# Kernel optimization log

Measured on AMD Instinct MI355X. Metric: run time of the kernel, lower is better.

The kernel has to match this reference:

```python
import jax, jax.numpy as jnp
import numpy as np

HIDDEN = 768  # hidden_dim of the embedding matrix
VOCAB = 30522


def setup_inputs() -> dict:
    key = jax.random.key(0)
    k1, k2, k3, k4, k5, k6 = jax.random.split(key, 6)
    core = jax.random.normal(k1, (40, 256, 256), dtype=jnp.float32)
    f0 = jax.random.normal(k2, (40, 40), dtype=jnp.float32)
    f1 = jax.random.normal(k3, (768, 256), dtype=jnp.float32)
    f2 = jax.random.normal(k4, (768, 256), dtype=jnp.float32)
    ids = jax.random.randint(k5, (8192,), 0, VOCAB, dtype=jnp.int32)
    x = jax.random.normal(k6, (8192, 768), dtype=jnp.float32)  # unused by forward, kept for signature parity
    return {"x": x, "ids": ids, "core": core, "f0": f0, "f1": f1, "f2": f2}


def reference(x, ids, core, f0, f1, f2):
    # tucker_to_tensor: core x_0 f0 x_1 f1 x_2 f2 -> (40, 768, 768)
    res = jnp.einsum('abc,ia,jb,kc->ijk', core, f0, f1, f2)
    # flatten to padded embedding table (30720, 768) and gather requested rows
    table = res.reshape(-1, HIDDEN)
    return table[ids, :]
```

## Files before the change

kernel.cpp:

```cpp
#include <hip/hip_runtime.h>


#define A_DIM 40
#define BC 65536
#define C_DIM 256
#define HID 768

typedef __attribute__((ext_vector_type(8))) short short8;
typedef __attribute__((ext_vector_type(4))) float floatx4;

#define AS1 __attribute__((address_space(1)))
#define AS3 __attribute__((address_space(3)))

__device__ __forceinline__ void gl2lds16(const unsigned short* g, unsigned short* l) {
    __builtin_amdgcn_global_load_lds((const AS1 unsigned int*)g, (AS3 unsigned int*)l,
                                     16, 0, 0);
}

__device__ __forceinline__ unsigned short f2bf(float f) {
    unsigned int u = __builtin_bit_cast(unsigned int, f);
    u += 0x7FFFu + ((u >> 16) & 1u);
    return (unsigned short)(u >> 16);
}

__global__ __launch_bounds__(256) void k01_fused(const float* __restrict__ core,
                                                 const float* __restrict__ f0,
                                                 const float* __restrict__ f1,
                                                 const float* __restrict__ f2,
                                                 unsigned short* __restrict__ A1t,
                                                 unsigned short* __restrict__ f1b,
                                                 unsigned short* __restrict__ f2b) {
    const int bid = blockIdx.x;
    const int tid = threadIdx.x;
    if (bid < 512) {
        __shared__ float f0s[200];
        __shared__ unsigned short tt[32 * 34];
        const int i0 = (bid >> 6) * 5;
        const int tile = bid & 63;
        const int b0 = (tile >> 3) * 32;
        const int c0 = (tile & 7) * 32;
        if (tid < 200) f0s[tid] = f0[i0 * A_DIM + tid];
        __syncthreads();

        const int pb = (tid >> 4) * 2;
        const int pc = (tid & 15) * 2;
        float acc[5][4];
#pragma unroll
        for (int ii = 0; ii < 5; ++ii)
#pragma unroll
            for (int e = 0; e < 4; ++e) acc[ii][e] = 0.f;

        const float* cp0 = core + (b0 + pb) * 256 + (c0 + pc);
        for (int a = 0; a < A_DIM; ++a) {
            const float* cp = cp0 + a * BC;
            const float2 r0 = *(const float2*)cp;
            const float2 r1 = *(const float2*)(cp + 256);
#pragma unroll
            for (int ii = 0; ii < 5; ++ii) {
                const float fa = f0s[ii * A_DIM + a];
                acc[ii][0] += fa * r0.x;
                acc[ii][1] += fa * r0.y;
                acc[ii][2] += fa * r1.x;
                acc[ii][3] += fa * r1.y;
            }
        }
        const int rc = tid >> 3;
        const int rb4 = (tid & 7) * 4;
#pragma unroll
        for (int ii = 0; ii < 5; ++ii) {
            if (ii) __syncthreads();
            unsigned short e00 = f2bf(acc[ii][0]);
            unsigned short e10 = f2bf(acc[ii][2]);
            unsigned short e01 = f2bf(acc[ii][1]);
            unsigned short e11 = f2bf(acc[ii][3]);
            *(unsigned int*)&tt[pc * 34 + pb]       = (unsigned int)e00 | ((unsigned int)e10 << 16);
            *(unsigned int*)&tt[(pc + 1) * 34 + pb] = (unsigned int)e01 | ((unsigned int)e11 << 16);
            __syncthreads();
            unsigned short o[4];
#pragma unroll
            for (int u = 0; u < 4; ++u) o[u] = tt[rc * 34 + rb4 + u];
            unsigned int lo = (unsigned int)o[0] | ((unsigned int)o[1] << 16);
            unsigned int hi = (unsigned int)o[2] | ((unsigned int)o[3] << 16);
            *(uint2*)&A1t[(size_t)(i0 + ii) * BC + (c0 + rc) * 256 + b0 + rb4] = make_uint2(lo, hi);
        }
    } else {
        const int idx = (bid - 512) * 256 + tid;
        const float* src;
        unsigned short* dst;
        int off;
        if (idx < 49152) { src = f1; dst = f1b; off = idx; }
        else             { src = f2; dst = f2b; off = idx - 49152; }
        const float4 v = *(const float4*)&src[off * 4];
        const unsigned int lo = (unsigned int)f2bf(v.x) | ((unsigned int)f2bf(v.y) << 16);
        const unsigned int hi = (unsigned int)f2bf(v.z) | ((unsigned int)f2bf(v.w) << 16);
        *(uint2*)&dst[off * 4] = make_uint2(lo, hi);
    }
}

__global__ __launch_bounds__(256) void k2_gemm(const unsigned short* __restrict__ f1b,
                                               const unsigned short* __restrict__ A1t,
                                               unsigned short* __restrict__ A2) {
    const int j0  = blockIdx.x * 128;
    const int cb0 = blockIdx.y * 128;

    __shared__ unsigned short As[128 * 32];
    __shared__ unsigned short Bs[128 * 32];

    const int tid = threadIdx.x;
    const int lane = tid & 63, wave = tid >> 6;
    const int wm = (wave >> 1) * 64, wn = (wave & 1) * 64;
    const int l16 = lane & 15, q = lane >> 4;

    floatx4 acc[4][4];
#pragma unroll
    for (int p = 0; p < 4; ++p)
#pragma unroll
        for (int r = 0; r < 4; ++r) acc[p][r] = (floatx4)0.f;

    for (int kk = 0; kk < C_DIM; kk += 32) {
#pragma unroll
        for (int u = 0; u < 2; ++u) {
            const int chunk = (wave * 2 + u) * 64 + lane;
            const int row = chunk >> 2;
            const int sl  = (chunk & 3) * 8;
            gl2lds16(&f1b[(j0 + row) * 256 + kk + sl],                 &As[(wave * 2 + u) * 512]);
            gl2lds16(&A1t[(size_t)(cb0 + row) * 256 + kk + sl],        &Bs[(wave * 2 + u) * 512]);
        }
        __syncthreads();
        short8 af[4], bf[4];
#pragma unroll
        for (int p = 0; p < 4; ++p) af[p] = *(const short8*)&As[(wm + p * 16 + l16) * 32 + q * 8];
#pragma unroll
        for (int r = 0; r < 4; ++r) bf[r] = *(const short8*)&Bs[(wn + r * 16 + l16) * 32 + q * 8];
#pragma unroll
        for (int p = 0; p < 4; ++p)
#pragma unroll
            for (int r = 0; r < 4; ++r)
                acc[p][r] = __builtin_amdgcn_mfma_f32_16x16x32_bf16(af[p], bf[r], acc[p][r], 0, 0, 0);
        __syncthreads();
    }
#pragma unroll
    for (int p = 0; p < 4; ++p)
#pragma unroll
        for (int r = 0; r < 4; ++r) {
            const int col = cb0 + wn + r * 16 + l16;
            const size_t base = (size_t)(col >> 8) * (768 * 256) + (size_t)(col & 255);
#pragma unroll
            for (int rr = 0; rr < 4; ++rr) {
                const int row = j0 + wm + p * 16 + q * 4 + rr;
                A2[base + (size_t)row * 256] = f2bf(acc[p][r][rr]);
            }
        }
}

__global__ __launch_bounds__(256) void k3_gemm(const unsigned short* __restrict__ A2,
                                               const unsigned short* __restrict__ f2b,
                                               const int* __restrict__ ids,
                                               float* __restrict__ out) {
    const int n0 = blockIdx.x * 128;
    const int k0 = blockIdx.y * 128;

    __shared__ int ids_s[128];
    __shared__ unsigned short As[128 * 32];
    __shared__ unsigned short Bs[128 * 32];

    const int tid = threadIdx.x;
    if (tid < 128) ids_s[tid] = ids[n0 + tid];
    __syncthreads();

    const int lane = tid & 63, wave = tid >> 6;
    const int wm = (wave >> 1) * 64, wn = (wave & 1) * 64;
    const int l16 = lane & 15, q = lane >> 4;

    floatx4 acc[4][4];
#pragma unroll
    for (int p = 0; p < 4; ++p)
#pragma unroll
        for (int r = 0; r < 4; ++r) acc[p][r] = (floatx4)0.f;

    for (int kk = 0; kk < C_DIM; kk += 32) {
#pragma unroll
        for (int u = 0; u < 2; ++u) {
            const int chunk = (wave * 2 + u) * 64 + lane;
            const int row = chunk >> 2;
            const int sl  = (chunk & 3) * 8;
            gl2lds16(&A2[(size_t)ids_s[row] * 256 + kk + sl],   &As[(wave * 2 + u) * 512]);
            gl2lds16(&f2b[(k0 + row) * 256 + kk + sl],          &Bs[(wave * 2 + u) * 512]);
        }
        __syncthreads();
        short8 af[4], bf[4];
#pragma unroll
        for (int p = 0; p < 4; ++p) af[p] = *(const short8*)&As[(wm + p * 16 + l16) * 32 + q * 8];
#pragma unroll
        for (int r = 0; r < 4; ++r) bf[r] = *(const short8*)&Bs[(wn + r * 16 + l16) * 32 + q * 8];
#pragma unroll
        for (int p = 0; p < 4; ++p)
#pragma unroll
            for (int r = 0; r < 4; ++r)
                acc[p][r] = __builtin_amdgcn_mfma_f32_16x16x32_bf16(af[p], bf[r], acc[p][r], 0, 0, 0);
        __syncthreads();
    }
#pragma unroll
    for (int p = 0; p < 4; ++p)
#pragma unroll
        for (int r = 0; r < 4; ++r)
#pragma unroll
            for (int rr = 0; rr < 4; ++rr) {
                const int row = n0 + wm + p * 16 + q * 4 + rr;
                const int col = k0 + wn + r * 16 + l16;
                out[(size_t)row * HID + col] = acc[p][r][rr];
            }
}

extern "C" void kernel_launch(void* const* d_in, const int* in_sizes, int n_in,
                              void* d_out, int out_size, void* d_ws, size_t ws_size,
                              hipStream_t stream) {
    const int*   ids  = (const int*)d_in[1];
    const float* core = (const float*)d_in[2];
    const float* f0   = (const float*)d_in[3];
    const float* f1   = (const float*)d_in[4];
    const float* f2   = (const float*)d_in[5];
    float* out = (float*)d_out;

    char* ws = (char*)d_ws;
    unsigned short* A1t = (unsigned short*)ws;
    unsigned short* A2  = (unsigned short*)(ws + 5242880);
    unsigned short* f1b = (unsigned short*)(ws + 20971520);
    unsigned short* f2b = (unsigned short*)(ws + 21364736);

    k01_fused<<<896, 256, 0, stream>>>(core, f0, f1, f2, A1t, f1b, f2b);
    k2_gemm<<<dim3(6, 80), 256, 0, stream>>>(f1b, A1t, A2);
    k3_gemm<<<dim3(64, 6), 256, 0, stream>>>(A2, f2b, ids, out);
}
```

Before: 112.0 us.

## Double-buffer LDS tiles with async prefetch in both bf16 GEMM kernels

Both MFMA GEMM kernels (k2_gemm and k3_gemm) now keep two LDS buffers per operand. The next K-slice is issued via global_load_lds while MFMAs run on the current slice. The per-iteration pair of __syncthreads is replaced by one vmcnt(0) wait plus an s_barrier, the loop is fully unrolled, and global addresses (including the id-gathered rows in k3) are precomputed once. This is meant to hide global-load latency behind compute, at the cost of doubling the LDS footprint, which may reduce occupancy.

```diff
diff --git a/kernel.cpp b/kernel.cpp
--- a/kernel.cpp
+++ b/kernel.cpp
@@ -21,6 +21,12 @@
     unsigned int u = __builtin_bit_cast(unsigned int, f);
     u += 0x7FFFu + ((u >> 16) & 1u);
     return (unsigned short)(u >> 16);
+}
+
+__device__ __forceinline__ void dma_barrier() {
+    asm volatile("s_waitcnt vmcnt(0)" ::: "memory");
+    __builtin_amdgcn_s_barrier();
+    __builtin_amdgcn_sched_barrier(0);
 }
 
 __global__ __launch_bounds__(256) void k01_fused(const float* __restrict__ core,
@@ -103,42 +109,56 @@
     const int j0  = blockIdx.x * 128;
     const int cb0 = blockIdx.y * 128;
 
-    __shared__ unsigned short As[128 * 32];
-    __shared__ unsigned short Bs[128 * 32];
+    __shared__ unsigned short As[2][128 * 32];
+    __shared__ unsigned short Bs[2][128 * 32];
 
     const int tid = threadIdx.x;
     const int lane = tid & 63, wave = tid >> 6;
     const int wm = (wave >> 1) * 64, wn = (wave & 1) * 64;
     const int l16 = lane & 15, q = lane >> 4;
 
+    const int ch0 = wave * 128 + lane;
+    const int ro0 = ch0 >> 2, sl0 = (ch0 & 3) * 8;
+    const int ch1 = ch0 + 64;
+    const int ro1 = ch1 >> 2, sl1 = (ch1 & 3) * 8;
+    const unsigned short* gA0 = &f1b[(j0 + ro0) * 256 + sl0];
+    const unsigned short* gA1 = &f1b[(j0 + ro1) * 256 + sl1];
+    const unsigned short* gB0 = &A1t[(size_t)(cb0 + ro0) * 256 + sl0];
+    const unsigned short* gB1 = &A1t[(size_t)(cb0 + ro1) * 256 + sl1];
+
+#define K2_STAGE(buf, kk)                                          \
+    do {                                                           \
+        gl2lds16(gA0 + (kk), &As[buf][(wave * 2 + 0) * 512]);      \
+        gl2lds16(gB0 + (kk), &Bs[buf][(wave * 2 + 0) * 512]);      \
+        gl2lds16(gA1 + (kk), &As[buf][(wave * 2 + 1) * 512]);      \
+        gl2lds16(gB1 + (kk), &Bs[buf][(wave * 2 + 1) * 512]);      \
+    } while (0)
+
     floatx4 acc[4][4];
 #pragma unroll
     for (int p = 0; p < 4; ++p)
 #pragma unroll
         for (int r = 0; r < 4; ++r) acc[p][r] = (floatx4)0.f;
 
-    for (int kk = 0; kk < C_DIM; kk += 32) {
-#pragma unroll
-        for (int u = 0; u < 2; ++u) {
-            const int chunk = (wave * 2 + u) * 64 + lane;
-            const int row = chunk >> 2;
-            const int sl  = (chunk & 3) * 8;
-            gl2lds16(&f1b[(j0 + row) * 256 + kk + sl],                 &As[(wave * 2 + u) * 512]);
-            gl2lds16(&A1t[(size_t)(cb0 + row) * 256 + kk + sl],        &Bs[(wave * 2 + u) * 512]);
-        }
-        __syncthreads();
-        short8 af[4], bf[4];
-#pragma unroll
-        for (int p = 0; p < 4; ++p) af[p] = *(const short8*)&As[(wm + p * 16 + l16) * 32 + q * 8];
-#pragma unroll
-        for (int r = 0; r < 4; ++r) bf[r] = *(const short8*)&Bs[(wn + r * 16 + l16) * 32 + q * 8];
+    K2_STAGE(0, 0);
+    dma_barrier();
+#pragma unroll
+    for (int t = 0; t < 8; ++t) {
+        const int cur = t & 1;
+        if (t < 7) K2_STAGE(cur ^ 1, (t + 1) * 32);
+        short8 af[4], bq[4];
+#pragma unroll
+        for (int p = 0; p < 4; ++p) af[p] = *(const short8*)&As[cur][(wm + p * 16 + l16) * 32 + q * 8];
+#pragma unroll
+        for (int r = 0; r < 4; ++r) bq[r] = *(const short8*)&Bs[cur][(wn + r * 16 + l16) * 32 + q * 8];
 #pragma unroll
         for (int p = 0; p < 4; ++p)
 #pragma unroll
             for (int r = 0; r < 4; ++r)
-                acc[p][r] = __builtin_amdgcn_mfma_f32_16x16x32_bf16(af[p], bf[r], acc[p][r], 0, 0, 0);
-        __syncthreads();
+                acc[p][r] = __builtin_amdgcn_mfma_f32_16x16x32_bf16(af[p], bq[r], acc[p][r], 0, 0, 0);
+        if (t < 7) dma_barrier();
     }
+#undef K2_STAGE
 #pragma unroll
     for (int p = 0; p < 4; ++p)
 #pragma unroll
@@ -161,8 +181,8 @@
     const int k0 = blockIdx.y * 128;
 
     __shared__ int ids_s[128];
-    __shared__ unsigned short As[128 * 32];
-    __shared__ unsigned short Bs[128 * 32];
+    __shared__ unsigned short As[2][128 * 32];
+    __shared__ unsigned short Bs[2][128 * 32];
 
     const int tid = threadIdx.x;
     if (tid < 128) ids_s[tid] = ids[n0 + tid];
@@ -172,34 +192,48 @@
     const int wm = (wave >> 1) * 64, wn = (wave & 1) * 64;
     const int l16 = lane & 15, q = lane >> 4;
 
+    const int ch0 = wave * 128 + lane;
+    const int ro0 = ch0 >> 2, sl0 = (ch0 & 3) * 8;
+    const int ch1 = ch0 + 64;
+    const int ro1 = ch1 >> 2, sl1 = (ch1 & 3) * 8;
+    const unsigned short* gA0 = &A2[(size_t)ids_s[ro0] * 256 + sl0];
+    const unsigned short* gA1 = &A2[(size_t)ids_s[ro1] * 256 + sl1];
+    const unsigned short* gB0 = &f2b[(k0 + ro0) * 256 + sl0];
+    const unsigned short* gB1 = &f2b[(k0 + ro1) * 256 + sl1];
+
+#define K3_STAGE(buf, kk)                                          \
+    do {                                                           \
+        gl2lds16(gA0 + (kk), &As[buf][(wave * 2 + 0) * 512]);      \
+        gl2lds16(gB0 + (kk), &Bs[buf][(wave * 2 + 0) * 512]);      \
+        gl2lds16(gA1 + (kk), &As[buf][(wave * 2 + 1) * 512]);      \
+        gl2lds16(gB1 + (kk), &Bs[buf][(wave * 2 + 1) * 512]);      \
+    } while (0)
+
     floatx4 acc[4][4];
 #pragma unroll
     for (int p = 0; p < 4; ++p)
 #pragma unroll
         for (int r = 0; r < 4; ++r) acc[p][r] = (floatx4)0.f;
 
-    for (int kk = 0; kk < C_DIM; kk += 32) {
-#pragma unroll
-        for (int u = 0; u < 2; ++u) {
-            const int chunk = (wave * 2 + u) * 64 + lane;
-            const int row = chunk >> 2;
-            const int sl  = (chunk & 3) * 8;
-            gl2lds16(&A2[(size_t)ids_s[row] * 256 + kk + sl],   &As[(wave * 2 + u) * 512]);
-            gl2lds16(&f2b[(k0 + row) * 256 + kk + sl],          &Bs[(wave * 2 + u) * 512]);
-        }
-        __syncthreads();
-        short8 af[4], bf[4];
-#pragma unroll
-        for (int p = 0; p < 4; ++p) af[p] = *(const short8*)&As[(wm + p * 16 + l16) * 32 + q * 8];
-#pragma unroll
-        for (int r = 0; r < 4; ++r) bf[r] = *(const short8*)&Bs[(wn + r * 16 + l16) * 32 + q * 8];
+    K3_STAGE(0, 0);
+    dma_barrier();
+#pragma unroll
+    for (int t = 0; t < 8; ++t) {
+        const int cur = t & 1;
+        if (t < 7) K3_STAGE(cur ^ 1, (t + 1) * 32);
+        short8 af[4], bq[4];
+#pragma unroll
+        for (int p = 0; p < 4; ++p) af[p] = *(const short8*)&As[cur][(wm + p * 16 + l16) * 32 + q * 8];
+#pragma unroll
+        for (int r = 0; r < 4; ++r) bq[r] = *(const short8*)&Bs[cur][(wn + r * 16 + l16) * 32 + q * 8];
 #pragma unroll
         for (int p = 0; p < 4; ++p)
 #pragma unroll
             for (int r = 0; r < 4; ++r)
-                acc[p][r] = __builtin_amdgcn_mfma_f32_16x16x32_bf16(af[p], bf[r], acc[p][r], 0, 0, 0);
-        __syncthreads();
+                acc[p][r] = __builtin_amdgcn_mfma_f32_16x16x32_bf16(af[p], bq[r], acc[p][r], 0, 0, 0);
+        if (t < 7) dma_barrier();
     }
+#undef K3_STAGE
 #pragma unroll
     for (int p = 0; p < 4; ++p)
 #pragma unroll
```

Result: slower. 114.5 us (+2.2%).
